# Kernel optimization log

Hardware: AMD Instinct MI355X
Metric: run time of the kernel (lower is better)

Reference implementation:

```python
import jax, jax.numpy as jnp
import numpy as np

R_SELF = 0.1  # config.r_self from the 'GENERAL' preset


def setup_inputs() -> dict:
    key = jax.random.key(0)
    k1, k2 = jax.random.split(key)
    N, M, D = 16384, 8192, 128
    x = jax.random.uniform(k1, (N, D), dtype=jnp.float32)
    self_samples = jax.random.uniform(k2, (M, D), dtype=jnp.float32)
    return {"x": x, "self_samples": self_samples}


def _cdist(a, b):
    # Euclidean pairwise distances, same math as torch.cdist(p=2).
    a2 = jnp.sum(a * a, axis=1, keepdims=True)          # [N,1]
    b2 = jnp.sum(b * b, axis=1)[None, :]                # [1,M]
    d2 = a2 + b2 - 2.0 * (a @ b.T)                      # [N,M]
    return jnp.sqrt(jnp.maximum(d2, 0.0))


def reference(x, self_samples):
    # get_anomaly_score: min over self set, shifted by r_self, clamped at 0.
    min_dist_to_self = jnp.min(_cdist(x, self_samples), axis=1)  # [N]
    score = jnp.maximum(min_dist_to_self - R_SELF, 0.0)
    return score
```

## Files before the change

### kernel.cpp

```cpp
#include <hip/hip_runtime.h>


using half_t = _Float16;
typedef _Float16 half8 __attribute__((ext_vector_type(8)));
typedef float floatx16 __attribute__((ext_vector_type(16)));

#define TILE_ELEMS (128 * 128)

__device__ __forceinline__ void async_load16(const void* g, void* l) {
    __builtin_amdgcn_global_load_lds(
        (const __attribute__((address_space(1))) void*)g,
        (__attribute__((address_space(3))) void*)l, 16, 0, 0);
}

__device__ __forceinline__ void stage_tile(const half_t* __restrict__ Bt,
                                           half_t* __restrict__ dst, int tid) {
    #pragma unroll
    for (int j = 0; j < 4; ++j) {
        int chunk = j * 512 + tid;
        async_load16(Bt + (size_t)chunk * 8, dst + (size_t)chunk * 8);
    }
}

__global__ __launch_bounds__(256) void prep_kernel(
    const float* __restrict__ x, const float* __restrict__ self,
    half_t* __restrict__ Aws, half_t* __restrict__ Bws,
    float* __restrict__ b2h, float* __restrict__ a2, int Atiles)
{
    __shared__ float part[256];
    int tile = blockIdx.x;
    int tid  = threadIdx.x;
    bool isB = tile >= Atiles;
    int bt   = tile - Atiles;
    const float* src = isB ? (self + (size_t)bt * TILE_ELEMS)
                           : (x    + (size_t)tile * TILE_ELEMS);
    half_t* dst = isB ? (Bws + (size_t)bt * TILE_ELEMS)
                      : (Aws + (size_t)tile * TILE_ELEMS);
    float sgn = isB ? 1.f : -1.f;

    int rowt = tid & 127;
    int k8b  = tid >> 7;
    float ss = 0.f;
    #pragma unroll
    for (int i = 0; i < 8; ++i) {
        int k8 = i * 2 + k8b;
        const float4* p = (const float4*)(src + rowt * 128 + k8 * 8);
        float4 f0 = p[0];
        float4 f1 = p[1];
        half8 h;
        h[0] = (half_t)(sgn * f0.x); h[1] = (half_t)(sgn * f0.y);
        h[2] = (half_t)(sgn * f0.z); h[3] = (half_t)(sgn * f0.w);
        h[4] = (half_t)(sgn * f1.x); h[5] = (half_t)(sgn * f1.y);
        h[6] = (half_t)(sgn * f1.z); h[7] = (half_t)(sgn * f1.w);
        *(half8*)(dst + (size_t)(i * 256 + tid) * 8) = h;
        ss += f0.x*f0.x + f0.y*f0.y + f0.z*f0.z + f0.w*f0.w;
        ss += f1.x*f1.x + f1.y*f1.y + f1.z*f1.z + f1.w*f1.w;
    }
    part[tid] = ss;
    __syncthreads();
    if (tid < 128) {
        float tot = part[tid] + part[tid + 128];
        if (isB) b2h[bt * 128 + tid] = 0.5f * tot;
        else     a2[tile * 128 + tid] = tot;
    }
}

template<int VN>
__device__ __forceinline__ void gemm_iter(
    int t, int iters, int tid, int wc, int ln31, int lh,
    const half_t* __restrict__ Bbase, half_t (*ring)[TILE_ELEMS],
    const float* __restrict__ b2sh,
    const half8 (&areg)[2][8], float (&minacc)[2][16])
{
    __builtin_amdgcn_sched_barrier(0);
    if constexpr (VN == 4) asm volatile("s_waitcnt vmcnt(4)" ::: "memory");
    else                   asm volatile("s_waitcnt vmcnt(0)" ::: "memory");
    asm volatile("s_waitcnt lgkmcnt(0)" ::: "memory");
    __builtin_amdgcn_s_barrier();
    __builtin_amdgcn_sched_barrier(0);

    if (t + 2 < iters)
        stage_tile(Bbase + (size_t)(t + 2) * TILE_ELEMS, &ring[(t + 2) % 3][0], tid);

    const half_t* Bs = &ring[t % 3][0];
    float b2v0 = b2sh[t * 128 + wc * 64 + ln31];
    float b2v1 = b2sh[t * 128 + wc * 64 + 32 + ln31];

    floatx16 c0, c1;
    #pragma unroll
    for (int r = 0; r < 16; ++r) { c0[r] = b2v0; c1[r] = b2v1; }

    floatx16 acc00, acc01, acc10, acc11;
    {
        half8 bf0 = *(const half8*)(Bs + (size_t)(lh * 128 + wc * 64 + ln31) * 8);
        half8 bf1 = *(const half8*)(Bs + (size_t)(lh * 128 + wc * 64 + 32 + ln31) * 8);
        acc00 = __builtin_amdgcn_mfma_f32_32x32x16_f16(areg[0][0], bf0, c0, 0, 0, 0);
        acc01 = __builtin_amdgcn_mfma_f32_32x32x16_f16(areg[0][0], bf1, c1, 0, 0, 0);
        acc10 = __builtin_amdgcn_mfma_f32_32x32x16_f16(areg[1][0], bf0, c0, 0, 0, 0);
        acc11 = __builtin_amdgcn_mfma_f32_32x32x16_f16(areg[1][0], bf1, c1, 0, 0, 0);
    }
    #pragma unroll
    for (int ki = 1; ki < 8; ++ki) {
        half8 bf0 = *(const half8*)(Bs + (size_t)((ki * 2 + lh) * 128 + wc * 64 + ln31) * 8);
        half8 bf1 = *(const half8*)(Bs + (size_t)((ki * 2 + lh) * 128 + wc * 64 + 32 + ln31) * 8);
        acc00 = __builtin_amdgcn_mfma_f32_32x32x16_f16(areg[0][ki], bf0, acc00, 0, 0, 0);
        acc01 = __builtin_amdgcn_mfma_f32_32x32x16_f16(areg[0][ki], bf1, acc01, 0, 0, 0);
        acc10 = __builtin_amdgcn_mfma_f32_32x32x16_f16(areg[1][ki], bf0, acc10, 0, 0, 0);
        acc11 = __builtin_amdgcn_mfma_f32_32x32x16_f16(areg[1][ki], bf1, acc11, 0, 0, 0);
    }

    #pragma unroll
    for (int r = 0; r < 16; ++r) {
        minacc[0][r] = fminf(fminf(acc00[r], acc01[r]), minacc[0][r]);
        minacc[1][r] = fminf(fminf(acc10[r], acc11[r]), minacc[1][r]);
    }
}

__global__ __launch_bounds__(512, 2) void min_gemm_kernel(
    const half_t* __restrict__ Aws, const half_t* __restrict__ Bws,
    const float* __restrict__ b2h, float* __restrict__ Pmin, int Mslice)
{
    __shared__ half_t ring[3][TILE_ELEMS];
    __shared__ float  b2sh[2048];

    int tid  = threadIdx.x;
    int lane = tid & 63;
    int wid  = tid >> 6;
    int wr   = wid >> 1, wc = wid & 1;
    int ln31 = lane & 31, lh = lane >> 5;

    const half_t* Atile = Aws + (size_t)(blockIdx.x * 2 + (wr >> 1)) * TILE_ELEMS;
    int rbase = (wr & 1) * 64;
    half8 areg[2][8];
    #pragma unroll
    for (int rt = 0; rt < 2; ++rt)
        #pragma unroll
        for (int ki = 0; ki < 8; ++ki)
            areg[rt][ki] = *(const half8*)(
                Atile + (size_t)((ki * 2 + lh) * 128 + rbase + rt * 32 + ln31) * 8);

    int s = blockIdx.y;
    for (int j = tid; j < Mslice; j += 512)
        b2sh[j] = b2h[s * Mslice + j];

    float minacc[2][16];
    #pragma unroll
    for (int rt = 0; rt < 2; ++rt)
        #pragma unroll
        for (int r = 0; r < 16; ++r) minacc[rt][r] = 1e30f;

    int iters = Mslice >> 7;
    const half_t* Bbase = Bws + (size_t)s * iters * TILE_ELEMS;

    __syncthreads();

    stage_tile(Bbase,              &ring[0][0], tid);
    stage_tile(Bbase + TILE_ELEMS, &ring[1][0], tid);

    for (int t = 0; t < iters - 1; ++t)
        gemm_iter<4>(t, iters, tid, wc, ln31, lh, Bbase, ring, b2sh, areg, minacc);
    gemm_iter<0>(iters - 1, iters, tid, wc, ln31, lh, Bbase, ring, b2sh, areg, minacc);

    #pragma unroll
    for (int rt = 0; rt < 2; ++rt)
        #pragma unroll
        for (int r = 0; r < 16; ++r) {
            float v = minacc[rt][r];
            #pragma unroll
            for (int m = 1; m < 32; m <<= 1)
                v = fminf(v, __shfl_xor(v, m, 64));
            if (ln31 == 0) {
                int row = blockIdx.x * 256 + wr * 64 + rt * 32
                        + (r & 3) + 8 * (r >> 2) + 4 * lh;
                Pmin[(size_t)row * 8 + s * 2 + wc] = v;
            }
        }
}

__global__ __launch_bounds__(256) void final_kernel(
    const float* __restrict__ a2, const float* __restrict__ Pmin,
    float* __restrict__ out)
{
    int row = blockIdx.x * 256 + threadIdx.x;
    const float4* pp = (const float4*)(Pmin + (size_t)row * 8);
    float4 p0 = pp[0];
    float4 p1 = pp[1];
    float p = fminf(fminf(fminf(p0.x, p0.y), fminf(p0.z, p0.w)),
                    fminf(fminf(p1.x, p1.y), fminf(p1.z, p1.w)));
    float d2 = a2[row] + 2.f * p;
    float d  = sqrtf(fmaxf(d2, 0.f));
    out[row] = fmaxf(d - 0.1f, 0.f);
}

extern "C" void kernel_launch(void* const* d_in, const int* in_sizes, int n_in,
                              void* d_out, int out_size, void* d_ws, size_t ws_size,
                              hipStream_t stream)
{
    const float* x    = (const float*)d_in[0];
    const float* self = (const float*)d_in[1];
    float* out        = (float*)d_out;

    int N = in_sizes[0] / 128;
    int M = in_sizes[1] / 128;
    int Atiles = N / 128;
    int Btiles = M / 128;

    char* w      = (char*)d_ws;
    half_t* Aws  = (half_t*)w;
    half_t* Bws  = Aws + (size_t)N * 128;
    float*  b2h  = (float*)(w + (size_t)(N + M) * 128 * 2);
    float*  Pmin = b2h + M;
    float*  a2   = Pmin + (size_t)N * 8;

    prep_kernel<<<Atiles + Btiles, 256, 0, stream>>>(x, self, Aws, Bws, b2h, a2, Atiles);

    int Mslice = M / 4;
    dim3 grid(N / 256, 4);
    min_gemm_kernel<<<grid, 512, 0, stream>>>(Aws, Bws, b2h, Pmin, Mslice);

    final_kernel<<<N / 256, 256, 0, stream>>>(a2, Pmin, out);
}
```

Measured before the change: 100.2 us.

## Retile waves to 128x32 per wave and keep running minimum in packed fp16

Measured after the change: 103.0 us. 2.9% more time.

```diff
diff --git a/kernel.cpp b/kernel.cpp
--- a/kernel.cpp
+++ b/kernel.cpp
@@ -3,6 +3,7 @@
 
 using half_t = _Float16;
 typedef _Float16 half8 __attribute__((ext_vector_type(8)));
+typedef _Float16 half2v __attribute__((ext_vector_type(2)));
 typedef float floatx16 __attribute__((ext_vector_type(16)));
 
 #define TILE_ELEMS (128 * 128)
@@ -20,6 +21,15 @@
         int chunk = j * 512 + tid;
         async_load16(Bt + (size_t)chunk * 8, dst + (size_t)chunk * 8);
     }
+}
+
+__device__ __forceinline__ half2v h2min(half2v a, half2v b) {
+    return __builtin_elementwise_min(a, b);
+}
+
+__device__ __forceinline__ half2v pkrtz(float lo, float hi) {
+    auto t = __builtin_amdgcn_cvt_pkrtz(lo, hi);
+    return __builtin_bit_cast(half2v, t);
 }
 
 __global__ __launch_bounds__(256) void prep_kernel(
@@ -70,7 +80,7 @@
     int t, int iters, int tid, int wc, int ln31, int lh,
     const half_t* __restrict__ Bbase, half_t (*ring)[TILE_ELEMS],
     const float* __restrict__ b2sh,
-    const half8 (&areg)[2][8], float (&minacc)[2][16])
+    const half8 (&areg)[4][8], half2v (&minacc)[4][8])
 {
     __builtin_amdgcn_sched_barrier(0);
     if constexpr (VN == 4) asm volatile("s_waitcnt vmcnt(4)" ::: "memory");
@@ -83,36 +93,31 @@
         stage_tile(Bbase + (size_t)(t + 2) * TILE_ELEMS, &ring[(t + 2) % 3][0], tid);
 
     const half_t* Bs = &ring[t % 3][0];
-    float b2v0 = b2sh[t * 128 + wc * 64 + ln31];
-    float b2v1 = b2sh[t * 128 + wc * 64 + 32 + ln31];
-
-    floatx16 c0, c1;
-    #pragma unroll
-    for (int r = 0; r < 16; ++r) { c0[r] = b2v0; c1[r] = b2v1; }
-
-    floatx16 acc00, acc01, acc10, acc11;
-    {
-        half8 bf0 = *(const half8*)(Bs + (size_t)(lh * 128 + wc * 64 + ln31) * 8);
-        half8 bf1 = *(const half8*)(Bs + (size_t)(lh * 128 + wc * 64 + 32 + ln31) * 8);
-        acc00 = __builtin_amdgcn_mfma_f32_32x32x16_f16(areg[0][0], bf0, c0, 0, 0, 0);
-        acc01 = __builtin_amdgcn_mfma_f32_32x32x16_f16(areg[0][0], bf1, c1, 0, 0, 0);
-        acc10 = __builtin_amdgcn_mfma_f32_32x32x16_f16(areg[1][0], bf0, c0, 0, 0, 0);
-        acc11 = __builtin_amdgcn_mfma_f32_32x32x16_f16(areg[1][0], bf1, c1, 0, 0, 0);
-    }
-    #pragma unroll
-    for (int ki = 1; ki < 8; ++ki) {
-        half8 bf0 = *(const half8*)(Bs + (size_t)((ki * 2 + lh) * 128 + wc * 64 + ln31) * 8);
-        half8 bf1 = *(const half8*)(Bs + (size_t)((ki * 2 + lh) * 128 + wc * 64 + 32 + ln31) * 8);
-        acc00 = __builtin_amdgcn_mfma_f32_32x32x16_f16(areg[0][ki], bf0, acc00, 0, 0, 0);
-        acc01 = __builtin_amdgcn_mfma_f32_32x32x16_f16(areg[0][ki], bf1, acc01, 0, 0, 0);
-        acc10 = __builtin_amdgcn_mfma_f32_32x32x16_f16(areg[1][ki], bf0, acc10, 0, 0, 0);
-        acc11 = __builtin_amdgcn_mfma_f32_32x32x16_f16(areg[1][ki], bf1, acc11, 0, 0, 0);
-    }
-
-    #pragma unroll
-    for (int r = 0; r < 16; ++r) {
-        minacc[0][r] = fminf(fminf(acc00[r], acc01[r]), minacc[0][r]);
-        minacc[1][r] = fminf(fminf(acc10[r], acc11[r]), minacc[1][r]);
+    float b2v = b2sh[t * 128 + wc * 32 + ln31];
+
+    half8 bf[8];
+    #pragma unroll
+    for (int ki = 0; ki < 8; ++ki)
+        bf[ki] = *(const half8*)(Bs + (size_t)((ki * 2 + lh) * 128 + wc * 32 + ln31) * 8);
+
+    floatx16 c0;
+    #pragma unroll
+    for (int r = 0; r < 16; ++r) c0[r] = b2v;
+
+    #pragma unroll
+    for (int rp = 0; rp < 2; ++rp) {
+        floatx16 a0 = __builtin_amdgcn_mfma_f32_32x32x16_f16(areg[rp * 2][0],     bf[0], c0, 0, 0, 0);
+        floatx16 a1 = __builtin_amdgcn_mfma_f32_32x32x16_f16(areg[rp * 2 + 1][0], bf[0], c0, 0, 0, 0);
+        #pragma unroll
+        for (int ki = 1; ki < 8; ++ki) {
+            a0 = __builtin_amdgcn_mfma_f32_32x32x16_f16(areg[rp * 2][ki],     bf[ki], a0, 0, 0, 0);
+            a1 = __builtin_amdgcn_mfma_f32_32x32x16_f16(areg[rp * 2 + 1][ki], bf[ki], a1, 0, 0, 0);
+        }
+        #pragma unroll
+        for (int i = 0; i < 8; ++i) {
+            minacc[rp * 2][i]     = h2min(minacc[rp * 2][i],     pkrtz(a0[2 * i], a0[2 * i + 1]));
+            minacc[rp * 2 + 1][i] = h2min(minacc[rp * 2 + 1][i], pkrtz(a1[2 * i], a1[2 * i + 1]));
+        }
     }
 }
 
@@ -126,28 +131,29 @@
     int tid  = threadIdx.x;
     int lane = tid & 63;
     int wid  = tid >> 6;
-    int wr   = wid >> 1, wc = wid & 1;
+    int wr   = wid >> 2;
+    int wc   = wid & 3;
     int ln31 = lane & 31, lh = lane >> 5;
 
-    const half_t* Atile = Aws + (size_t)(blockIdx.x * 2 + (wr >> 1)) * TILE_ELEMS;
-    int rbase = (wr & 1) * 64;
-    half8 areg[2][8];
-    #pragma unroll
-    for (int rt = 0; rt < 2; ++rt)
+    const half_t* Atile = Aws + (size_t)(blockIdx.x * 2 + wr) * TILE_ELEMS;
+    half8 areg[4][8];
+    #pragma unroll
+    for (int rt = 0; rt < 4; ++rt)
         #pragma unroll
         for (int ki = 0; ki < 8; ++ki)
             areg[rt][ki] = *(const half8*)(
-                Atile + (size_t)((ki * 2 + lh) * 128 + rbase + rt * 32 + ln31) * 8);
+                Atile + (size_t)((ki * 2 + lh) * 128 + rt * 32 + ln31) * 8);
 
     int s = blockIdx.y;
     for (int j = tid; j < Mslice; j += 512)
         b2sh[j] = b2h[s * Mslice + j];
 
-    float minacc[2][16];
-    #pragma unroll
-    for (int rt = 0; rt < 2; ++rt)
-        #pragma unroll
-        for (int r = 0; r < 16; ++r) minacc[rt][r] = 1e30f;
+    half2v minacc[4][8];
+    const half_t HMAX = (half_t)65504.f;
+    #pragma unroll
+    for (int rt = 0; rt < 4; ++rt)
+        #pragma unroll
+        for (int i = 0; i < 8; ++i) { minacc[rt][i][0] = HMAX; minacc[rt][i][1] = HMAX; }
 
     int iters = Mslice >> 7;
     const half_t* Bbase = Bws + (size_t)s * iters * TILE_ELEMS;
@@ -162,17 +168,25 @@
     gemm_iter<0>(iters - 1, iters, tid, wc, ln31, lh, Bbase, ring, b2sh, areg, minacc);
 
     #pragma unroll
-    for (int rt = 0; rt < 2; ++rt)
-        #pragma unroll
-        for (int r = 0; r < 16; ++r) {
-            float v = minacc[rt][r];
+    for (int rt = 0; rt < 4; ++rt)
+        #pragma unroll
+        for (int i = 0; i < 8; ++i) {
+            int m = __builtin_bit_cast(int, minacc[rt][i]);
             #pragma unroll
-            for (int m = 1; m < 32; m <<= 1)
-                v = fminf(v, __shfl_xor(v, m, 64));
+            for (int x = 1; x < 32; x <<= 1) {
+                int o = __shfl_xor(m, x, 64);
+                m = __builtin_bit_cast(int,
+                        h2min(__builtin_bit_cast(half2v, m),
+                              __builtin_bit_cast(half2v, o)));
+            }
             if (ln31 == 0) {
-                int row = blockIdx.x * 256 + wr * 64 + rt * 32
-                        + (r & 3) + 8 * (r >> 2) + 4 * lh;
-                Pmin[(size_t)row * 8 + s * 2 + wc] = v;
+                half2v mv = __builtin_bit_cast(half2v, m);
+                int r0 = 2 * i, r1 = 2 * i + 1;
+                int rowb = blockIdx.x * 256 + wr * 128 + rt * 32 + 4 * lh;
+                int row0 = rowb + (r0 & 3) + 8 * (r0 >> 2);
+                int row1 = rowb + (r1 & 3) + 8 * (r1 >> 2);
+                Pmin[(size_t)row0 * 16 + s * 4 + wc] = (float)mv[0];
+                Pmin[(size_t)row1 * 16 + s * 4 + wc] = (float)mv[1];
             }
         }
 }
@@ -182,11 +196,16 @@
     float* __restrict__ out)
 {
     int row = blockIdx.x * 256 + threadIdx.x;
-    const float4* pp = (const float4*)(Pmin + (size_t)row * 8);
+    const float4* pp = (const float4*)(Pmin + (size_t)row * 16);
     float4 p0 = pp[0];
     float4 p1 = pp[1];
-    float p = fminf(fminf(fminf(p0.x, p0.y), fminf(p0.z, p0.w)),
-                    fminf(fminf(p1.x, p1.y), fminf(p1.z, p1.w)));
+    float4 p2 = pp[2];
+    float4 p3 = pp[3];
+    float q0 = fminf(fminf(p0.x, p0.y), fminf(p0.z, p0.w));
+    float q1 = fminf(fminf(p1.x, p1.y), fminf(p1.z, p1.w));
+    float q2 = fminf(fminf(p2.x, p2.y), fminf(p2.z, p2.w));
+    float q3 = fminf(fminf(p3.x, p3.y), fminf(p3.z, p3.w));
+    float p  = fminf(fminf(q0, q1), fminf(q2, q3));
     float d2 = a2[row] + 2.f * p;
     float d  = sqrtf(fmaxf(d2, 0.f));
     out[row] = fmaxf(d - 0.1f, 0.f);
@@ -210,7 +229,7 @@
     half_t* Bws  = Aws + (size_t)N * 128;
     float*  b2h  = (float*)(w + (size_t)(N + M) * 128 * 2);
     float*  Pmin = b2h + M;
-    float*  a2   = Pmin + (size_t)N * 8;
+    float*  a2   = Pmin + (size_t)N * 16;
 
     prep_kernel<<<Atiles + Btiles, 256, 0, stream>>>(x, self, Aws, Bws, b2h, a2, Atiles);
 
```

## Replace 3-deep single-tile ring with double-buffered two-tile epochs

Applied to the files above, without the earlier changes.

After: 100.5 us. Within noise of the previous version (+0.3%).

```diff
diff --git a/kernel.cpp b/kernel.cpp
--- a/kernel.cpp
+++ b/kernel.cpp
@@ -13,12 +13,12 @@
         (__attribute__((address_space(3))) void*)l, 16, 0, 0);
 }
 
-__device__ __forceinline__ void stage_tile(const half_t* __restrict__ Bt,
-                                           half_t* __restrict__ dst, int tid) {
-    #pragma unroll
-    for (int j = 0; j < 4; ++j) {
-        int chunk = j * 512 + tid;
-        async_load16(Bt + (size_t)chunk * 8, dst + (size_t)chunk * 8);
+__device__ __forceinline__ void stage_epoch(const half_t* __restrict__ Bt,
+                                            half_t* __restrict__ dst, int tid) {
+    #pragma unroll
+    for (int p = 0; p < 8; ++p) {
+        int c = p * 512 + tid;
+        async_load16(Bt + (size_t)c * 8, dst + (size_t)c * 8);
     }
 }
 
@@ -65,62 +65,11 @@
     }
 }
 
-template<int VN>
-__device__ __forceinline__ void gemm_iter(
-    int t, int iters, int tid, int wc, int ln31, int lh,
-    const half_t* __restrict__ Bbase, half_t (*ring)[TILE_ELEMS],
-    const float* __restrict__ b2sh,
-    const half8 (&areg)[2][8], float (&minacc)[2][16])
-{
-    __builtin_amdgcn_sched_barrier(0);
-    if constexpr (VN == 4) asm volatile("s_waitcnt vmcnt(4)" ::: "memory");
-    else                   asm volatile("s_waitcnt vmcnt(0)" ::: "memory");
-    asm volatile("s_waitcnt lgkmcnt(0)" ::: "memory");
-    __builtin_amdgcn_s_barrier();
-    __builtin_amdgcn_sched_barrier(0);
-
-    if (t + 2 < iters)
-        stage_tile(Bbase + (size_t)(t + 2) * TILE_ELEMS, &ring[(t + 2) % 3][0], tid);
-
-    const half_t* Bs = &ring[t % 3][0];
-    float b2v0 = b2sh[t * 128 + wc * 64 + ln31];
-    float b2v1 = b2sh[t * 128 + wc * 64 + 32 + ln31];
-
-    floatx16 c0, c1;
-    #pragma unroll
-    for (int r = 0; r < 16; ++r) { c0[r] = b2v0; c1[r] = b2v1; }
-
-    floatx16 acc00, acc01, acc10, acc11;
-    {
-        half8 bf0 = *(const half8*)(Bs + (size_t)(lh * 128 + wc * 64 + ln31) * 8);
-        half8 bf1 = *(const half8*)(Bs + (size_t)(lh * 128 + wc * 64 + 32 + ln31) * 8);
-        acc00 = __builtin_amdgcn_mfma_f32_32x32x16_f16(areg[0][0], bf0, c0, 0, 0, 0);
-        acc01 = __builtin_amdgcn_mfma_f32_32x32x16_f16(areg[0][0], bf1, c1, 0, 0, 0);
-        acc10 = __builtin_amdgcn_mfma_f32_32x32x16_f16(areg[1][0], bf0, c0, 0, 0, 0);
-        acc11 = __builtin_amdgcn_mfma_f32_32x32x16_f16(areg[1][0], bf1, c1, 0, 0, 0);
-    }
-    #pragma unroll
-    for (int ki = 1; ki < 8; ++ki) {
-        half8 bf0 = *(const half8*)(Bs + (size_t)((ki * 2 + lh) * 128 + wc * 64 + ln31) * 8);
-        half8 bf1 = *(const half8*)(Bs + (size_t)((ki * 2 + lh) * 128 + wc * 64 + 32 + ln31) * 8);
-        acc00 = __builtin_amdgcn_mfma_f32_32x32x16_f16(areg[0][ki], bf0, acc00, 0, 0, 0);
-        acc01 = __builtin_amdgcn_mfma_f32_32x32x16_f16(areg[0][ki], bf1, acc01, 0, 0, 0);
-        acc10 = __builtin_amdgcn_mfma_f32_32x32x16_f16(areg[1][ki], bf0, acc10, 0, 0, 0);
-        acc11 = __builtin_amdgcn_mfma_f32_32x32x16_f16(areg[1][ki], bf1, acc11, 0, 0, 0);
-    }
-
-    #pragma unroll
-    for (int r = 0; r < 16; ++r) {
-        minacc[0][r] = fminf(fminf(acc00[r], acc01[r]), minacc[0][r]);
-        minacc[1][r] = fminf(fminf(acc10[r], acc11[r]), minacc[1][r]);
-    }
-}
-
 __global__ __launch_bounds__(512, 2) void min_gemm_kernel(
     const half_t* __restrict__ Aws, const half_t* __restrict__ Bws,
     const float* __restrict__ b2h, float* __restrict__ Pmin, int Mslice)
 {
-    __shared__ half_t ring[3][TILE_ELEMS];
+    __shared__ half_t dbuf[2][2 * TILE_ELEMS];
     __shared__ float  b2sh[2048];
 
     int tid  = threadIdx.x;
@@ -149,17 +98,63 @@
         #pragma unroll
         for (int r = 0; r < 16; ++r) minacc[rt][r] = 1e30f;
 
-    int iters = Mslice >> 7;
-    const half_t* Bbase = Bws + (size_t)s * iters * TILE_ELEMS;
+    int epochs = Mslice >> 8;
+    const half_t* Bbase = Bws + (size_t)s * (Mslice >> 7) * TILE_ELEMS;
 
     __syncthreads();
 
-    stage_tile(Bbase,              &ring[0][0], tid);
-    stage_tile(Bbase + TILE_ELEMS, &ring[1][0], tid);
-
-    for (int t = 0; t < iters - 1; ++t)
-        gemm_iter<4>(t, iters, tid, wc, ln31, lh, Bbase, ring, b2sh, areg, minacc);
-    gemm_iter<0>(iters - 1, iters, tid, wc, ln31, lh, Bbase, ring, b2sh, areg, minacc);
+    stage_epoch(Bbase, &dbuf[0][0], tid);
+
+    for (int e = 0; e < epochs; ++e) {
+        asm volatile("s_waitcnt vmcnt(0)" ::: "memory");
+        __builtin_amdgcn_sched_barrier(0);
+        __builtin_amdgcn_s_barrier();
+        __builtin_amdgcn_sched_barrier(0);
+
+        if (e + 1 < epochs)
+            stage_epoch(Bbase + (size_t)(2 * e + 2) * TILE_ELEMS,
+                        &dbuf[(e + 1) & 1][0], tid);
+
+        #pragma unroll
+        for (int sub = 0; sub < 2; ++sub) {
+            int t = 2 * e + sub;
+            const half_t* Bs = &dbuf[e & 1][0] + (size_t)sub * TILE_ELEMS;
+
+            float b2v0 = b2sh[t * 128 + wc * 64 + ln31];
+            float b2v1 = b2sh[t * 128 + wc * 64 + 32 + ln31];
+
+            floatx16 c0, c1;
+            #pragma unroll
+            for (int r = 0; r < 16; ++r) { c0[r] = b2v0; c1[r] = b2v1; }
+
+            floatx16 acc00, acc01, acc10, acc11;
+            {
+                int k8 = lh;
+                half8 bf0 = *(const half8*)(Bs + (size_t)(k8 * 128 + wc * 64 + ln31) * 8);
+                half8 bf1 = *(const half8*)(Bs + (size_t)(k8 * 128 + wc * 64 + 32 + ln31) * 8);
+                acc00 = __builtin_amdgcn_mfma_f32_32x32x16_f16(areg[0][0], bf0, c0, 0, 0, 0);
+                acc01 = __builtin_amdgcn_mfma_f32_32x32x16_f16(areg[0][0], bf1, c1, 0, 0, 0);
+                acc10 = __builtin_amdgcn_mfma_f32_32x32x16_f16(areg[1][0], bf0, c0, 0, 0, 0);
+                acc11 = __builtin_amdgcn_mfma_f32_32x32x16_f16(areg[1][0], bf1, c1, 0, 0, 0);
+            }
+            #pragma unroll
+            for (int ki = 1; ki < 8; ++ki) {
+                int k8 = ki * 2 + lh;
+                half8 bf0 = *(const half8*)(Bs + (size_t)(k8 * 128 + wc * 64 + ln31) * 8);
+                half8 bf1 = *(const half8*)(Bs + (size_t)(k8 * 128 + wc * 64 + 32 + ln31) * 8);
+                acc00 = __builtin_amdgcn_mfma_f32_32x32x16_f16(areg[0][ki], bf0, acc00, 0, 0, 0);
+                acc01 = __builtin_amdgcn_mfma_f32_32x32x16_f16(areg[0][ki], bf1, acc01, 0, 0, 0);
+                acc10 = __builtin_amdgcn_mfma_f32_32x32x16_f16(areg[1][ki], bf0, acc10, 0, 0, 0);
+                acc11 = __builtin_amdgcn_mfma_f32_32x32x16_f16(areg[1][ki], bf1, acc11, 0, 0, 0);
+            }
+
+            #pragma unroll
+            for (int r = 0; r < 16; ++r) {
+                minacc[0][r] = fminf(fminf(acc00[r], acc01[r]), minacc[0][r]);
+                minacc[1][r] = fminf(fminf(acc10[r], acc11[r]), minacc[1][r]);
+            }
+        }
+    }
 
     #pragma unroll
     for (int rt = 0; rt < 2; ++rt)
```
